# Optimization experiments

Measured on AMD Instinct MI355X. Metric: run time of the kernel, lower is better.

Reference implementation:

```python
import jax, jax.numpy as jnp
import numpy as np
from functools import partial

EPS = 1e-5
PATCH = 3
STYLE_STRENGTH = 1.0


def _whiten_color_mats(x):
    # x: (b, c, n) already flattened; returns mean, eigvecs, eigvals of covariance
    mean = x.mean(axis=-1, keepdims=True)
    xc = x - mean
    n = x.shape[-1]
    cov = jnp.einsum('bcn,bdn->bcd', xc, xc) / (n - 1)
    evals, evecs = jnp.linalg.eigh(cov)
    evals = jnp.maximum(evals, EPS)
    return mean, xc, evecs, evals


def whitening(x):
    b, c, h, w = x.shape
    xf = x.reshape(b, c, h * w)
    _, xc, E, d = _whiten_color_mats(xf)
    # W = E diag(d^-1/2) E^T
    Wm = jnp.einsum('bce,be,bde->bcd', E, d ** -0.5, E)
    return jnp.einsum('bcd,bdn->bcn', Wm, xc).reshape(b, c, h, w)


def coloring(x, style):
    b, c, h, w = x.shape
    xf = x.reshape(b, c, h * w)
    sf = style.reshape(b, c, -1)
    smean, sc, E, d = _whiten_color_mats(sf)
    Cm = jnp.einsum('bce,be,bde->bcd', E, d ** 0.5, E)
    out = jnp.einsum('bcd,bdn->bcn', Cm, xf) + smean
    return out.reshape(b, c, h, w)


def extract_style_kernels(style):
    # returns (b, hw, c, 3, 3) patches and (b, hw, 1, 1, 1) L2 norms
    b, c, H, W = style.shape
    p = jnp.pad(style, ((0, 0), (0, 0), (1, 1), (1, 1)), mode='reflect')
    patches = jnp.stack([p[:, :, i:i + H, j:j + W]
                         for i in range(PATCH) for j in range(PATCH)], axis=-1)  # (b,c,H,W,9)
    k = patches.reshape(b, c, H * W, PATCH * PATCH).transpose(0, 2, 1, 3)  # (b,hw,c,9)
    norm = jnp.sqrt(jnp.sum(k * k, axis=(2, 3))) + EPS  # (b,hw)
    return k.reshape(b, H * W, c, PATCH, PATCH), norm[:, :, None, None, None]


_DN = ('NCHW', 'OIHW', 'NCHW')


def _conv_per_sample(feat, kern):
    # feat (c,H,W), kern (o,c,3,3): reflect-pad 1, VALID conv -> (o,H,W)
    fp = jnp.pad(feat, ((0, 0), (1, 1), (1, 1)), mode='reflect')
    out = jax.lax.conv_general_dilated(fp[None], kern, (1, 1), 'VALID',
                                       dimension_numbers=_DN)
    return out[0]


def _deconv_per_sample(onehot, kern):
    # conv_transpose2d(stride=1, padding=2) == VALID conv with flipped, transposed kernel
    kt = jnp.flip(kern, axis=(-2, -1)).transpose(1, 0, 2, 3)  # (c, hw, 3, 3)
    fp = jnp.pad(onehot, ((0, 0), (1, 1), (1, 1)), mode='reflect')
    out = jax.lax.conv_general_dilated(fp[None], kt, (1, 1), 'VALID',
                                       dimension_numbers=_DN)
    return out[0]


def norm_deconvolution(h, w, patch_size):
    full = np.zeros((h + patch_size - 1, w + patch_size - 1), dtype=np.float32)
    for x in range(patch_size):
        for y in range(patch_size):
            full[y:y + h, x:x + w] += 1.0
    pw = (patch_size - 1) // 2
    if pw > 0:
        full = full[pw:-pw, pw:-pw]
    return jnp.asarray(full)[None, None]  # (1,1,h,w)


def reassemble_feature(nc, ns):
    b, c, H, W = nc.shape
    hw = H * W
    kern, norm = extract_style_kernels(ns)
    score = jax.vmap(_conv_per_sample)(nc, kern / norm)  # (b, hw, H, W)
    idx = jnp.argmax(score, axis=1)  # (b, H, W)
    onehot = (jnp.arange(hw, dtype=idx.dtype)[None, :, None, None] == idx[:, None]
              ).astype(nc.dtype)  # (b, hw, H, W)
    recon = jax.vmap(_deconv_per_sample)(onehot, kern)  # (b, c, H, W)
    return recon / norm_deconvolution(H, W, PATCH).astype(recon.dtype)


def setup_inputs() -> dict:
    key = jax.random.key(0)
    k1, k2 = jax.random.split(key)
    content_feature = jax.random.normal(k1, (2, 256, 64, 64), dtype=jnp.float32)
    style_feature = jax.random.normal(k2, (2, 256, 64, 64), dtype=jnp.float32)
    return {"content_feature": content_feature, "style_feature": style_feature}


def reference(content_feature, style_feature):
    nc = whitening(content_feature)
    ns = whitening(style_feature)
    reassembled = reassemble_feature(nc, ns)
    stylized = coloring(reassembled, style_feature)
    return (1.0 - STYLE_STRENGTH) * content_feature + STYLE_STRENGTH * stylized
```

## Files before the change

### kernel.cpp

```cpp
#include <hip/hip_runtime.h>
#include <hip/hip_bf16.h>

#define C_ 256
#define N_ 4096
#define CN (C_*N_)
#define EPSF 1e-5f
#define NS_ITERS 6
#define KSPLIT 16
#define LSTR 40

typedef _Float16 f16x8 __attribute__((ext_vector_type(8)));
typedef float f32x4 __attribute__((ext_vector_type(4)));

__device__ __forceinline__ int refl(int t) {
  return t < 0 ? -t : (t > 63 ? 126 - t : t);
}

__device__ __forceinline__ unsigned short f2h(float x) {
  _Float16 h = (_Float16)x;
  return __builtin_bit_cast(unsigned short, h);
}
__device__ __forceinline__ float h2f(unsigned short u) {
  return (float)__builtin_bit_cast(_Float16, u);
}

__device__ __forceinline__ void mm64_3term(unsigned short* sm, const float* A, const float* B,
                                           int m0, int n0, f32x4 acc[2][2]) {
  const int P = 64*LSTR;
  int t = threadIdx.x;
  int lane = t & 63;
  int wv = (t >> 7) & 1, wu = (t >> 6) & 1;
  int lx16 = lane & 15, quad = lane >> 4;
  int srow = t >> 2, sseg = (t & 3) * 8;
#pragma unroll
  for (int i = 0; i < 2; i++)
#pragma unroll
    for (int j = 0; j < 2; j++) acc[i][j] = (f32x4){0.f, 0.f, 0.f, 0.f};
  for (int k0 = 0; k0 < 256; k0 += 32) {
    __syncthreads();
    {
      const float* pa = &A[(size_t)(m0 + srow)*256 + k0 + sseg];
      const float* pb = &B[(size_t)(n0 + srow)*256 + k0 + sseg];
#pragma unroll
      for (int g = 0; g < 2; g++) {
        float4 va = *(const float4*)(pa + g*4);
        float4 vb = *(const float4*)(pb + g*4);
        float fa[4] = {va.x, va.y, va.z, va.w};
        float fb[4] = {vb.x, vb.y, vb.z, vb.w};
        unsigned short ha[4], la[4], hb[4], lb[4];
#pragma unroll
        for (int j = 0; j < 4; j++) {
          unsigned short h = f2h(fa[j]); ha[j] = h; la[j] = f2h(fa[j] - h2f(h));
          h = f2h(fb[j]); hb[j] = h; lb[j] = f2h(fb[j] - h2f(h));
        }
        int lo_ = srow*LSTR + sseg + g*4;
        *(ushort4*)&sm[0*P + lo_] = make_ushort4(ha[0], ha[1], ha[2], ha[3]);
        *(ushort4*)&sm[1*P + lo_] = make_ushort4(la[0], la[1], la[2], la[3]);
        *(ushort4*)&sm[2*P + lo_] = make_ushort4(hb[0], hb[1], hb[2], hb[3]);
        *(ushort4*)&sm[3*P + lo_] = make_ushort4(lb[0], lb[1], lb[2], lb[3]);
      }
    }
    __syncthreads();
    f16x8 ah[2], al[2], bh[2], bl[2];
#pragma unroll
    for (int mt = 0; mt < 2; mt++) {
      int arow = (wv*32 + mt*16 + lx16)*LSTR + quad*8;
      ah[mt] = *(const f16x8*)&sm[0*P + arow];
      al[mt] = *(const f16x8*)&sm[1*P + arow];
    }
#pragma unroll
    for (int nt = 0; nt < 2; nt++) {
      int brow = (wu*32 + nt*16 + lx16)*LSTR + quad*8;
      bh[nt] = *(const f16x8*)&sm[2*P + brow];
      bl[nt] = *(const f16x8*)&sm[3*P + brow];
    }
#pragma unroll
    for (int mt = 0; mt < 2; mt++)
#pragma unroll
      for (int nt = 0; nt < 2; nt++) {
        f32x4 a = acc[mt][nt];
        a = __builtin_amdgcn_mfma_f32_16x16x32_f16(ah[mt], bh[nt], a, 0, 0, 0);
        a = __builtin_amdgcn_mfma_f32_16x16x32_f16(ah[mt], bl[nt], a, 0, 0, 0);
        a = __builtin_amdgcn_mfma_f32_16x16x32_f16(al[mt], bh[nt], a, 0, 0, 0);
        acc[mt][nt] = a;
      }
  }
}

__device__ __forceinline__ f32x4 mm32_3term(unsigned short* sm, const float* A, const float* B,
                                            int m0, int n0) {
  const int P = 32*LSTR;
  int t = threadIdx.x, lane = t & 63;
  int w = t >> 6, wv = w >> 1, wu = w & 1;
  int lx16 = lane & 15, quad = lane >> 4;
  int mat = t >> 7, srow = (t >> 2) & 31, sseg = (t & 3) * 8;
  const float* S = mat ? B : A;
  int rb = mat ? n0 : m0;
  int base0 = mat ? 2*P : 0;
  f32x4 acc = (f32x4){0.f, 0.f, 0.f, 0.f};
  for (int k0 = 0; k0 < 256; k0 += 32) {
    __syncthreads();
    {
      const float* p = &S[(size_t)(rb + srow)*256 + k0 + sseg];
      int lo_ = srow*LSTR + sseg;
#pragma unroll
      for (int g = 0; g < 2; g++) {
        float4 v = *(const float4*)(p + g*4);
        float f[4] = {v.x, v.y, v.z, v.w};
        unsigned short hh[4], ll[4];
#pragma unroll
        for (int j = 0; j < 4; j++) {
          unsigned short h = f2h(f[j]); hh[j] = h; ll[j] = f2h(f[j] - h2f(h));
        }
        *(ushort4*)&sm[base0 + lo_ + g*4]     = make_ushort4(hh[0], hh[1], hh[2], hh[3]);
        *(ushort4*)&sm[base0 + P + lo_ + g*4] = make_ushort4(ll[0], ll[1], ll[2], ll[3]);
      }
    }
    __syncthreads();
    int arow = (wv*16 + lx16)*LSTR + quad*8;
    int brow = (wu*16 + lx16)*LSTR + quad*8;
    f16x8 ah = *(const f16x8*)&sm[0*P + arow];
    f16x8 al = *(const f16x8*)&sm[1*P + arow];
    f16x8 bh = *(const f16x8*)&sm[2*P + brow];
    f16x8 bl = *(const f16x8*)&sm[3*P + brow];
    acc = __builtin_amdgcn_mfma_f32_16x16x32_f16(ah, bh, acc, 0, 0, 0);
    acc = __builtin_amdgcn_mfma_f32_16x16x32_f16(ah, bl, acc, 0, 0, 0);
    acc = __builtin_amdgcn_mfma_f32_16x16x32_f16(al, bh, acc, 0, 0, 0);
  }
  return acc;
}

__global__ __launch_bounds__(256) void k_mean(const float* content, const float* style,
                                              float* means) {
  int c = blockIdx.x, m = blockIdx.y, t = threadIdx.x;
  const float* x = (m < 2 ? content : style) + (size_t)(m & 1) * CN + (size_t)c * N_;
  float s = 0.f;
  for (int i = t; i < N_; i += 256) s += x[i];
  __shared__ float red[256];
  red[t] = s; __syncthreads();
  for (int off = 128; off > 0; off >>= 1) { if (t < off) red[t] += red[t + off]; __syncthreads(); }
  if (t == 0) means[m * C_ + c] = red[0] * (1.f / N_);
}

__global__ __launch_bounds__(256) void k_splitall(const float* content, const float* style,
                                                  const float* means,
                                                  unsigned short* covsp, unsigned short* xcT) {
  int m = blockIdx.z;
  const float* x = (m < 2 ? content : style) + (size_t)(m & 1) * CN;
  int u0 = blockIdx.x * 32, c0 = blockIdx.y * 32;
  unsigned short* ch_ = covsp + (size_t)(2*m+0)*CN;
  unsigned short* cl_ = covsp + (size_t)(2*m+1)*CN;
  unsigned short* th_ = xcT + (size_t)(2*m+0)*CN;
  unsigned short* tl_ = xcT + (size_t)(2*m+1)*CN;
  __shared__ float tile[32][33];
  int t = threadIdx.x;
  {
    int cc = t >> 3, uu4 = (t & 7) * 4;
    float4 v = *(const float4*)&x[(size_t)(c0+cc)*N_ + u0 + uu4];
    float f[4] = {v.x, v.y, v.z, v.w};
    unsigned short h[4], lo[4];
#pragma unroll
    for (int j = 0; j < 4; j++) {
      unsigned short hh = f2h(f[j]);
      h[j] = hh; lo[j] = f2h(f[j] - h2f(hh));
      tile[cc][uu4+j] = f[j];
    }
    size_t o = (size_t)(c0+cc)*N_ + u0 + uu4;
    *(ushort4*)&ch_[o] = make_ushort4(h[0], h[1], h[2], h[3]);
    *(ushort4*)&cl_[o] = make_ushort4(lo[0], lo[1], lo[2], lo[3]);
  }
  __syncthreads();
  {
    int uu = t >> 3, cc4 = (t & 7) * 4;
    unsigned short h[4], lo[4];
#pragma unroll
    for (int j = 0; j < 4; j++) {
      float v = tile[cc4+j][uu] - means[m*C_ + c0 + cc4 + j];
      unsigned short hh = f2h(v);
      h[j] = hh; lo[j] = f2h(v - h2f(hh));
    }
    size_t o = (size_t)(u0+uu)*C_ + c0 + cc4;
    *(ushort4*)&th_[o] = make_ushort4(h[0], h[1], h[2], h[3]);
    *(ushort4*)&tl_[o] = make_ushort4(lo[0], lo[1], lo[2], lo[3]);
  }
}

__global__ __launch_bounds__(512) void k_covmm(const unsigned short* sp, float* covp) {
  __shared__ unsigned short sm[4*128*LSTR];
  const int P = 128*LSTR;
  int t = threadIdx.x;
  int kc = blockIdx.x, m = blockIdx.z;
  int ti = blockIdx.y >> 1, tj = blockIdx.y & 1;
  const unsigned short* Xh = sp + (size_t)m * 2 * (size_t)CN;
  const unsigned short* Xl = Xh + CN;
  int v0 = ti * 128, u0 = tj * 128;
  int wave = t >> 6, lane = t & 63;
  int wv = wave >> 1, wu = wave & 1;
  int lx16 = lane & 15, quad = lane >> 4;
  int srow = t >> 2, sseg = (t & 3) * 8;
  f32x4 acc[2][4];
#pragma unroll
  for (int i = 0; i < 2; i++)
#pragma unroll
    for (int j = 0; j < 4; j++) acc[i][j] = (f32x4){0.f, 0.f, 0.f, 0.f};

  int kbeg = kc * (N_ / KSPLIT), kend = kbeg + (N_ / KSPLIT);
  for (int k0 = kbeg; k0 < kend; k0 += 32) {
    __syncthreads();
    {
      size_t goA = (size_t)(v0 + srow) * N_ + k0 + sseg;
      size_t goB = (size_t)(u0 + srow) * N_ + k0 + sseg;
      int lo_ = srow * LSTR + sseg;
      *(float4*)&sm[0*P + lo_] = *(const float4*)&Xh[goA];
      *(float4*)&sm[1*P + lo_] = *(const float4*)&Xl[goA];
      *(float4*)&sm[2*P + lo_] = *(const float4*)&Xh[goB];
      *(float4*)&sm[3*P + lo_] = *(const float4*)&Xl[goB];
    }
    __syncthreads();
#pragma unroll
    for (int mt = 0; mt < 2; mt++) {
      int arow = (wv*32 + mt*16 + lx16)*LSTR + quad*8;
      f16x8 ah = *(const f16x8*)&sm[0*P + arow];
      f16x8 al = *(const f16x8*)&sm[1*P + arow];
#pragma unroll
      for (int nt = 0; nt < 4; nt++) {
        int brow = (wu*64 + nt*16 + lx16)*LSTR + quad*8;
        f16x8 bh = *(const f16x8*)&sm[2*P + brow];
        f16x8 bl = *(const f16x8*)&sm[3*P + brow];
        f32x4 a = acc[mt][nt];
        a = __builtin_amdgcn_mfma_f32_16x16x32_f16(ah, bh, a, 0, 0, 0);
        a = __builtin_amdgcn_mfma_f32_16x16x32_f16(ah, bl, a, 0, 0, 0);
        a = __builtin_amdgcn_mfma_f32_16x16x32_f16(al, bh, a, 0, 0, 0);
        acc[mt][nt] = a;
      }
    }
  }
  float* O = covp + ((size_t)kc*4 + m) * 65536;
#pragma unroll
  for (int mt = 0; mt < 2; mt++)
#pragma unroll
    for (int nt = 0; nt < 4; nt++)
#pragma unroll
      for (int i = 0; i < 4; i++)
        O[(size_t)(v0 + wv*32 + mt*16 + quad*4 + i)*C_ + (u0 + wu*64 + nt*16 + lx16)] =
            acc[mt][nt][i];
}

__global__ __launch_bounds__(256) void k_trace2(const float* covp, const float* means,
                                                float* cnrm) {
  int m = blockIdx.x, t = threadIdx.x;
  float s = 0.f;
#pragma unroll
  for (int kc = 0; kc < KSPLIT; kc++)
    s += covp[((size_t)kc*4 + m)*65536 + (size_t)t*257];
  float mi = means[m*C_ + t];
  float d = (s - (float)N_*mi*mi) * (1.f/(float)(N_-1));
  __shared__ float red[256];
  red[t] = d; __syncthreads();
  for (int off = 128; off > 0; off >>= 1) { if (t < off) red[t] += red[t + off]; __syncthreads(); }
  if (!t) cnrm[m] = red[0] * (1.3f/256.f);
}

__global__ __launch_bounds__(256) void k_covred_init(const float* covp, const float* means,
                                                     const float* cnrm, float* Y, float* Z) {
  int i = blockIdx.x, m = blockIdx.y, j = threadIdx.x;
  float s = 0.f;
#pragma unroll
  for (int kc = 0; kc < KSPLIT; kc++)
    s += covp[((size_t)kc*4 + m)*65536 + (size_t)i*C_ + j];
  float mi = means[m*C_ + i], mj = means[m*C_ + j];
  float cv = (s - (float)N_*mi*mj) * (1.f/(float)(N_-1));
  size_t o = (size_t)m*65536 + (size_t)i*C_ + j;
  Y[o] = cv / cnrm[m];
  Z[o] = (i == j) ? 1.f : 0.f;
}

__global__ __launch_bounds__(256) void k_nsA(const float* Zin, const float* Yin, float* T) {
  __shared__ unsigned short sm[4*32*LSTR];
  int m = blockIdx.y;
  int m0 = (blockIdx.x >> 3) * 32, n0 = (blockIdx.x & 7) * 32;
  const float* A = Zin + (size_t)m*65536;
  const float* B = Yin + (size_t)m*65536;
  float* O = T + (size_t)m*65536;
  f32x4 acc = mm32_3term(sm, A, B, m0, n0);
  int t = threadIdx.x, lane = t & 63;
  int w = t >> 6, wv = w >> 1, wu = w & 1;
  int lx16 = lane & 15, quad = lane >> 4;
#pragma unroll
  for (int i = 0; i < 4; i++) {
    int r = m0 + wv*16 + quad*4 + i;
    int c = n0 + wu*16 + lx16;
    float v = acc[i];
    O[(size_t)r*256 + c] = (r == c) ? 3.f - v : -v;
  }
}

__global__ __launch_bounds__(256) void k_nsB(const float* Yin, const float* Zin, const float* T,
                                             float* Yout, float* Zout) {
  __shared__ unsigned short sm[4*32*LSTR];
  int m = blockIdx.y, z = blockIdx.z;
  const float* A = (z == 0 ? Yin : Zin) + (size_t)m*65536;
  const float* B = T + (size_t)m*65536;
  float* O = (z == 0 ? Yout : Zout) + (size_t)m*65536;
  int m0 = (blockIdx.x >> 3) * 32, n0 = (blockIdx.x & 7) * 32;
  f32x4 acc = mm32_3term(sm, A, B, m0, n0);
  int t = threadIdx.x, lane = t & 63;
  int w = t >> 6, wv = w >> 1, wu = w & 1;
  int lx16 = lane & 15, quad = lane >> 4;
#pragma unroll
  for (int i = 0; i < 4; i++) {
    int r = m0 + wv*16 + quad*4 + i;
    int c = n0 + wu*16 + lx16;
    O[(size_t)r*256 + c] = 0.5f * acc[i];
  }
}

__global__ __launch_bounds__(256) void k_whitenT(const unsigned short* xcT, const float* Zall,
                                                 const float* cnrm, unsigned short* outT) {
  __shared__ unsigned short sm[4*64*LSTR];
  const int P = 64*LSTR;
  int m = blockIdx.z;
  int v0 = blockIdx.x * 64, c0 = blockIdx.y * 64;
  const float* Zm = Zall + (size_t)m*65536;
  const unsigned short* Bh_g = xcT + (size_t)(2*m+0)*CN;
  const unsigned short* Bl_g = xcT + (size_t)(2*m+1)*CN;
  unsigned short* Oh = outT + (size_t)(2*m+0)*CN;
  unsigned short* Ol = outT + (size_t)(2*m+1)*CN;
  int t = threadIdx.x, lane = t & 63;
  int wv = (t >> 7) & 1, wu = (t >> 6) & 1;
  int lx16 = lane & 15, quad = lane >> 4;
  int srow = t >> 2, sseg = (t & 3) * 8;
  f32x4 acc[2][2];
#pragma unroll
  for (int i = 0; i < 2; i++)
#pragma unroll
    for (int j = 0; j < 2; j++) acc[i][j] = (f32x4){0.f, 0.f, 0.f, 0.f};
  for (int k0 = 0; k0 < 256; k0 += 32) {
    __syncthreads();
    {
      const float* pa = &Zm[(size_t)(c0 + srow)*256 + k0 + sseg];
      int lo_ = srow*LSTR + sseg;
#pragma unroll
      for (int g = 0; g < 2; g++) {
        float4 va = *(const float4*)(pa + g*4);
        float fa[4] = {va.x, va.y, va.z, va.w};
        unsigned short ha[4], la[4];
#pragma unroll
        for (int j = 0; j < 4; j++) {
          unsigned short h = f2h(fa[j]); ha[j] = h; la[j] = f2h(fa[j] - h2f(h));
        }
        *(ushort4*)&sm[0*P + lo_ + g*4] = make_ushort4(ha[0], ha[1], ha[2], ha[3]);
        *(ushort4*)&sm[1*P + lo_ + g*4] = make_ushort4(la[0], la[1], la[2], la[3]);
      }
      size_t gb = (size_t)(v0 + srow)*C_ + k0 + sseg;
      *(float4*)&sm[2*P + lo_] = *(const float4*)&Bh_g[gb];
      *(float4*)&sm[3*P + lo_] = *(const float4*)&Bl_g[gb];
    }
    __syncthreads();
    f16x8 ah[2], al[2], bh[2], bl[2];
#pragma unroll
    for (int mt = 0; mt < 2; mt++) {
      int arow = (wv*32 + mt*16 + lx16)*LSTR + quad*8;
      ah[mt] = *(const f16x8*)&sm[0*P + arow];
      al[mt] = *(const f16x8*)&sm[1*P + arow];
    }
#pragma unroll
    for (int nt = 0; nt < 2; nt++) {
      int brow = (wu*32 + nt*16 + lx16)*LSTR + quad*8;
      bh[nt] = *(const f16x8*)&sm[2*P + brow];
      bl[nt] = *(const f16x8*)&sm[3*P + brow];
    }
#pragma unroll
    for (int mt = 0; mt < 2; mt++)
#pragma unroll
      for (int nt = 0; nt < 2; nt++) {
        f32x4 a = acc[mt][nt];
        a = __builtin_amdgcn_mfma_f32_16x16x32_f16(ah[mt], bh[nt], a, 0, 0, 0);
        a = __builtin_amdgcn_mfma_f32_16x16x32_f16(ah[mt], bl[nt], a, 0, 0, 0);
        a = __builtin_amdgcn_mfma_f32_16x16x32_f16(al[mt], bh[nt], a, 0, 0, 0);
        acc[mt][nt] = a;
      }
  }
  float scale = 1.0f / sqrtf(cnrm[m]);
  __syncthreads();
  unsigned short* Th = sm;
  unsigned short* Tl = sm + 64*72;
#pragma unroll
  for (int mt = 0; mt < 2; mt++)
#pragma unroll
    for (int nt = 0; nt < 2; nt++)
#pragma unroll
      for (int i = 0; i < 4; i++) {
        int chl = wv*32 + mt*16 + quad*4 + i;
        int vl  = wu*32 + nt*16 + lx16;
        float w = acc[mt][nt][i] * scale;
        unsigned short h = f2h(w);
        unsigned short l = f2h(w - h2f(h));
        Th[vl*72 + chl] = h;
        Tl[vl*72 + chl] = l;
      }
  __syncthreads();
  int vr = t >> 2, cs = (t & 3) * 16;
  size_t go = (size_t)(v0 + vr)*C_ + c0 + cs;
  *(float4*)&Oh[go]     = *(float4*)&Th[vr*72 + cs];
  *(float4*)&Oh[go + 8] = *(float4*)&Th[vr*72 + cs + 8];
  *(float4*)&Ol[go]     = *(float4*)&Tl[vr*72 + cs];
  *(float4*)&Ol[go + 8] = *(float4*)&Tl[vr*72 + cs + 8];
}

__global__ __launch_bounds__(256) void k_ssq(const unsigned short* outT, float* ssq) {
  int b = blockIdx.y; int p = blockIdx.x * 256 + threadIdx.x;
  const unsigned short* h = outT + (size_t)(2*(2+b))*CN + (size_t)p*C_;
  const unsigned short* l = h + CN;
  float acc = 0.f;
  for (int c = 0; c < C_; c += 4) {
    ushort4 hv = *(const ushort4*)&h[c];
    ushort4 lv = *(const ushort4*)&l[c];
    float v0 = h2f(hv.x) + h2f(lv.x);
    float v1 = h2f(hv.y) + h2f(lv.y);
    float v2 = h2f(hv.z) + h2f(lv.z);
    float v3 = h2f(hv.w) + h2f(lv.w);
    acc += v0*v0 + v1*v1 + v2*v2 + v3*v3;
  }
  ssq[b*N_ + p] = acc;
}

__global__ __launch_bounds__(256) void k_rnorm(const float* ssq, float* rnorm) {
  int b = blockIdx.y; int s = blockIdx.x * 256 + threadIdx.x;
  int sy = s >> 6, sx = s & 63;
  float sum = 0.f;
#pragma unroll
  for (int ky = 0; ky < 3; ky++)
#pragma unroll
    for (int kx = 0; kx < 3; kx++)
      sum += ssq[b*N_ + refl(sy+ky-1)*64 + refl(sx+kx-1)];
  rnorm[b*N_ + s] = 1.f / (sqrtf(sum) + EPSF);
}

__global__ __launch_bounds__(512) void k_gram(const unsigned short* Ah_g, const unsigned short* Al_g,
                                              const unsigned short* Bh_g, const unsigned short* Bl_g,
                                              float* Hx) {
  __shared__ unsigned short sm[4*128*LSTR];
  const int P = 128*LSTR;
  int t = threadIdx.x;
  int v0 = blockIdx.y * 128, u0 = blockIdx.x * 128;
  int wave = t >> 6, lane = t & 63;
  int wv = wave >> 1, wu = wave & 1;
  int lx16 = lane & 15, quad = lane >> 4;
  int srow = t >> 2, sseg = (t & 3) * 8;
  f32x4 acc[2][4];
#pragma unroll
  for (int i = 0; i < 2; i++)
#pragma unroll
    for (int j = 0; j < 4; j++) acc[i][j] = (f32x4){0.f, 0.f, 0.f, 0.f};

  for (int k0 = 0; k0 < 256; k0 += 32) {
    __syncthreads();
    {
      size_t goA = (size_t)(v0 + srow)*C_ + k0 + sseg;
      size_t goB = (size_t)(u0 + srow)*C_ + k0 + sseg;
      int lo_ = srow*LSTR + sseg;
      *(float4*)&sm[0*P + lo_] = *(const float4*)&Ah_g[goA];
      *(float4*)&sm[1*P + lo_] = *(const float4*)&Al_g[goA];
      *(float4*)&sm[2*P + lo_] = *(const float4*)&Bh_g[goB];
      *(float4*)&sm[3*P + lo_] = *(const float4*)&Bl_g[goB];
    }
    __syncthreads();
    int kb = quad*8;
    f16x8 ah[2], al[2];
#pragma unroll
    for (int mt = 0; mt < 2; mt++) {
      int arow = (wv*32 + mt*16 + lx16)*LSTR + kb;
      ah[mt] = *(const f16x8*)&sm[0*P + arow];
      al[mt] = *(const f16x8*)&sm[1*P + arow];
    }
    f16x8 bh[4], bl[4];
#pragma unroll
    for (int nt = 0; nt < 4; nt++) {
      int brow = (wu*64 + nt*16 + lx16)*LSTR + kb;
      bh[nt] = *(const f16x8*)&sm[2*P + brow];
      bl[nt] = *(const f16x8*)&sm[3*P + brow];
    }
#pragma unroll
    for (int mt = 0; mt < 2; mt++)
#pragma unroll
      for (int nt = 0; nt < 4; nt++) {
        f32x4 a = acc[mt][nt];
        a = __builtin_amdgcn_mfma_f32_16x16x32_f16(ah[mt], bh[nt], a, 0, 0, 0);
        a = __builtin_amdgcn_mfma_f32_16x16x32_f16(ah[mt], bl[nt], a, 0, 0, 0);
        a = __builtin_amdgcn_mfma_f32_16x16x32_f16(al[mt], bh[nt], a, 0, 0, 0);
        acc[mt][nt] = a;
      }
  }
  float* Gs = (float*)sm;
  int btx = t & 15, bty = t >> 4;
#pragma unroll
  for (int h = 0; h < 2; h++) {
    __syncthreads();
    if ((wv >> 1) == h) {
      int rbase = (wv & 1) * 32;
#pragma unroll
      for (int mt = 0; mt < 2; mt++)
#pragma unroll
        for (int nt = 0; nt < 4; nt++)
#pragma unroll
          for (int i = 0; i < 4; i++)
            Gs[(rbase + mt*16 + quad*4 + i)*133 + wu*64 + nt*16 + lx16] = acc[mt][nt][i];
    }
    __syncthreads();
#pragma unroll
    for (int i = 0; i < 2; i++) {
      int px = bty + 32*i;
      int xm = refl(px-1), xp = refl(px+1);
#pragma unroll
      for (int jh = 0; jh < 2; jh++) {
        int ub = jh*64;
        float tmp[4];
#pragma unroll
        for (int j = 0; j < 4; j++) {
          int sx = btx*4 + j;
          int smm = refl(sx-1), sp = refl(sx+1);
          tmp[j] = Gs[xm*133 + ub + smm] + Gs[px*133 + ub + sx] + Gs[xp*133 + ub + sp];
        }
        *(float4*)&Hx[(size_t)(v0 + h*64 + px)*N_ + u0 + ub + btx*4] =
            make_float4(tmp[0], tmp[1], tmp[2], tmp[3]);
      }
    }
  }
}

__global__ __launch_bounds__(256) void k_argmax(const float* Hx, const float* rnorm,
                                                int* idx, int b) {
  int blk = blockIdx.x, t = threadIdx.x;
  int q = blk >> 6, px = blk & 63;
  int py0 = 2*q, py1 = 2*q + 1;
  size_t rm = (size_t)(refl(py0-1)*64 + px) * N_;
  size_t r0 = (size_t)(py0*64 + px) * N_;
  size_t r1 = (size_t)(py1*64 + px) * N_;
  size_t rp = (size_t)(refl(py1+1)*64 + px) * N_;
  float bv0 = -1e30f, bv1 = -1e30f; int bs0 = 0, bs1 = 0;
  for (int s = t; s < N_; s += 256) {
    int sy = s >> 6, sx = s & 63;
    int u0 = refl(sy-1)*64 + sx, u2 = refl(sy+1)*64 + sx;
    float rn = rnorm[b*N_ + s];
    float a0 = Hx[rm + u0] + Hx[r0 + s] + Hx[r1 + u2];
    float a1 = Hx[r0 + u0] + Hx[r1 + s] + Hx[rp + u2];
    float sc0 = a0 * rn, sc1 = a1 * rn;
    if (sc0 > bv0) { bv0 = sc0; bs0 = s; }
    if (sc1 > bv1) { bv1 = sc1; bs1 = s; }
  }
  __shared__ float sv[256]; __shared__ int si[256];
  sv[t] = bv0; si[t] = bs0; __syncthreads();
  for (int off = 128; off > 0; off >>= 1) {
    if (t < off) {
      if (sv[t+off] > sv[t] || (sv[t+off] == sv[t] && si[t+off] < si[t])) {
        sv[t] = sv[t+off]; si[t] = si[t+off];
      }
    }
    __syncthreads();
  }
  if (!t) idx[b*N_ + py0*64 + px] = si[0];
  __syncthreads();
  sv[t] = bv1; si[t] = bs1; __syncthreads();
  for (int off = 128; off > 0; off >>= 1) {
    if (t < off) {
      if (sv[t+off] > sv[t] || (sv[t+off] == sv[t] && si[t+off] < si[t])) {
        sv[t] = sv[t+off]; si[t] = si[t+off];
      }
    }
    __syncthreads();
  }
  if (!t) idx[b*N_ + py1*64 + px] = si[0];
}

__global__ __launch_bounds__(256) void k_recon(const unsigned short* nsTh,
                                               const unsigned short* nsTl,
                                               const int* idx_b, float* recont_b) {
  int p = blockIdx.x, c = threadIdx.x;
  int py = p >> 6, px = p & 63;
  float acc = 0.f;
#pragma unroll
  for (int dy = 0; dy < 3; dy++)
#pragma unroll
    for (int dx = 0; dx < 3; dx++) {
      int q = refl(py+dy-1)*64 + refl(px+dx-1);
      int s = idx_b[q];
      int sy = s >> 6, sx = s & 63;
      size_t o = (size_t)(refl(sy+1-dy)*64 + refl(sx+1-dx))*C_ + c;
      acc += h2f(nsTh[o]) + h2f(nsTl[o]);
    }
  float dc = ((py==0||py==63)?2.f:3.f) * ((px==0||px==63)?2.f:3.f);
  recont_b[(size_t)p*C_ + c] = acc / dc;
}

__global__ __launch_bounds__(256) void k_color(const float* Yall, const float* recont_all,
                                               const float* cnrm, const float* means,
                                               float* out_all) {
  __shared__ unsigned short sm[4*64*LSTR];
  int b = blockIdx.z;
  const float* Ym = Yall + (size_t)(2+b)*65536;
  const float* recont = recont_all + (size_t)b*CN;
  const float* smean = means + (2+b)*C_;
  float* out = out_all + (size_t)b*CN;
  int m0 = blockIdx.y * 64;
  int n0 = blockIdx.x * 64;
  f32x4 acc[2][2];
  mm64_3term(sm, Ym, recont, m0, n0, acc);
  float scale = sqrtf(cnrm[2+b]);
  int t = threadIdx.x, lane = t & 63;
  int wv = (t >> 7) & 1, wu = (t >> 6) & 1, lx16 = lane & 15, quad = lane >> 4;
#pragma unroll
  for (int mt = 0; mt < 2; mt++)
#pragma unroll
    for (int nt = 0; nt < 2; nt++)
#pragma unroll
      for (int i = 0; i < 4; i++) {
        int r = m0 + wv*32 + mt*16 + quad*4 + i;
        int c = n0 + wu*32 + nt*16 + lx16;
        out[(size_t)r*N_ + c] = acc[mt][nt][i]*scale + smean[r];
      }
}

extern "C" void kernel_launch(void* const* d_in, const int* in_sizes, int n_in,
                              void* d_out, int out_size, void* d_ws, size_t ws_size,
                              hipStream_t stream) {
  const float* content = (const float*)d_in[0];
  const float* style   = (const float*)d_in[1];
  float* out = (float*)d_out;

  float* F = (float*)d_ws;
  float* means  = F + 0;
  float* cnrm   = F + 1024;
  float* Y      = F + 264192;
  float* Z      = F + 526336;
  float* Y2     = F + 788480;
  float* Z2     = F + 1050624;
  float* T      = F + 1312768;
  float* ncreg  = F + 1574912;
  float* nsreg  = F + 3672064;
  float* recont = F + 7866368;
  float* ssq    = F + 9963520;
  float* rnorm  = F + 9971712;
  int*   idx    = (int*)(F + 9979904);
  float* Hx     = F + 9988096;

  unsigned short* covsp = (unsigned short*)Hx;
  float* covp = Hx + 4194304;

  unsigned short* xcT  = (unsigned short*)nsreg;
  unsigned short* outT = (unsigned short*)ncreg;

  k_mean<<<dim3(256,4), 256, 0, stream>>>(content, style, means);
  k_splitall<<<dim3(128,8,4), 256, 0, stream>>>(content, style, means, covsp, xcT);
  k_covmm<<<dim3(KSPLIT,4,4), 512, 0, stream>>>(covsp, covp);
  k_trace2<<<4, 256, 0, stream>>>(covp, means, cnrm);
  k_covred_init<<<dim3(256,4), 256, 0, stream>>>(covp, means, cnrm, Y, Z);
  float *Ya = Y, *Za = Z, *Yb = Y2, *Zb = Z2;
  for (int it = 0; it < NS_ITERS; it++) {
    k_nsA<<<dim3(64,4), 256, 0, stream>>>(Za, Ya, T);
    k_nsB<<<dim3(64,4,2), 256, 0, stream>>>(Ya, Za, T, Yb, Zb);
    float* tmp;
    tmp = Ya; Ya = Yb; Yb = tmp;
    tmp = Za; Za = Zb; Zb = tmp;
  }
  k_whitenT<<<dim3(64,4,4), 256, 0, stream>>>(xcT, Za, cnrm, outT);
  k_ssq<<<dim3(16,2), 256, 0, stream>>>(outT, ssq);
  k_rnorm<<<dim3(16,2), 256, 0, stream>>>(ssq, rnorm);
  for (int b = 0; b < 2; b++) {
    k_gram<<<dim3(32,32), 512, 0, stream>>>(outT + (size_t)(2*b)*CN,
                                            outT + (size_t)(2*b+1)*CN,
                                            outT + (size_t)(2*(2+b))*CN,
                                            outT + (size_t)(2*(2+b)+1)*CN, Hx);
    k_argmax<<<2048, 256, 0, stream>>>(Hx, rnorm, idx, b);
    k_recon<<<4096, 256, 0, stream>>>(outT + (size_t)(2*(2+b))*CN,
                                      outT + (size_t)(2*(2+b)+1)*CN,
                                      idx + (size_t)b*N_, recont + (size_t)b*CN);
  }
  k_color<<<dim3(64,4,2), 256, 0, stream>>>(Ya, recont, cnrm, means, out);
}
```

Before: 351.8 us.

## Fuse Newton-Schulz iterations into cooperative kernel and widen argmax rows per block

Replaces the per-iteration Newton-Schulz kernel launches with one cooperative kernel that uses grid-wide syncs between phases. The argmax kernel now handles four output rows per block, so Hx rows shared between neighbours are reused. The covariance split-K factor is doubled and the mean kernel reads float4. The aim is less launch overhead and less redundant memory traffic. The cost is grid-sync overhead and a reliance on cooperative launch residency.

```diff
diff --git a/kernel.cpp b/kernel.cpp
--- a/kernel.cpp
+++ b/kernel.cpp
@@ -1,12 +1,15 @@
 #include <hip/hip_runtime.h>
 #include <hip/hip_bf16.h>
+#include <hip/hip_cooperative_groups.h>
+
+namespace cg = cooperative_groups;
 
 #define C_ 256
 #define N_ 4096
 #define CN (C_*N_)
 #define EPSF 1e-5f
 #define NS_ITERS 6
-#define KSPLIT 16
+#define KSPLIT 32
 #define LSTR 40
 
 typedef _Float16 f16x8 __attribute__((ext_vector_type(8)));
@@ -134,8 +137,13 @@
                                               float* means) {
   int c = blockIdx.x, m = blockIdx.y, t = threadIdx.x;
   const float* x = (m < 2 ? content : style) + (size_t)(m & 1) * CN + (size_t)c * N_;
+  const float4* x4 = (const float4*)x;
   float s = 0.f;
-  for (int i = t; i < N_; i += 256) s += x[i];
+#pragma unroll
+  for (int i = 0; i < 4; i++) {
+    float4 v = x4[t + i*256];
+    s += v.x + v.y + v.z + v.w;
+  }
   __shared__ float red[256];
   red[t] = s; __syncthreads();
   for (int off = 128; off > 0; off >>= 1) { if (t < off) red[t] += red[t + off]; __syncthreads(); }
@@ -275,43 +283,48 @@
   Z[o] = (i == j) ? 1.f : 0.f;
 }
 
-__global__ __launch_bounds__(256) void k_nsA(const float* Zin, const float* Yin, float* T) {
+__global__ __launch_bounds__(256) void k_ns_all(float* Y, float* Z, float* Y2, float* Z2,
+                                                float* T) {
+  cg::grid_group grid = cg::this_grid();
   __shared__ unsigned short sm[4*32*LSTR];
-  int m = blockIdx.y;
-  int m0 = (blockIdx.x >> 3) * 32, n0 = (blockIdx.x & 7) * 32;
-  const float* A = Zin + (size_t)m*65536;
-  const float* B = Yin + (size_t)m*65536;
-  float* O = T + (size_t)m*65536;
-  f32x4 acc = mm32_3term(sm, A, B, m0, n0);
+  int b = blockIdx.x;
   int t = threadIdx.x, lane = t & 63;
   int w = t >> 6, wv = w >> 1, wu = w & 1;
   int lx16 = lane & 15, quad = lane >> 4;
-#pragma unroll
-  for (int i = 0; i < 4; i++) {
-    int r = m0 + wv*16 + quad*4 + i;
-    int c = n0 + wu*16 + lx16;
-    float v = acc[i];
-    O[(size_t)r*256 + c] = (r == c) ? 3.f - v : -v;
-  }
-}
-
-__global__ __launch_bounds__(256) void k_nsB(const float* Yin, const float* Zin, const float* T,
-                                             float* Yout, float* Zout) {
-  __shared__ unsigned short sm[4*32*LSTR];
-  int m = blockIdx.y, z = blockIdx.z;
-  const float* A = (z == 0 ? Yin : Zin) + (size_t)m*65536;
-  const float* B = T + (size_t)m*65536;
-  float* O = (z == 0 ? Yout : Zout) + (size_t)m*65536;
-  int m0 = (blockIdx.x >> 3) * 32, n0 = (blockIdx.x & 7) * 32;
-  f32x4 acc = mm32_3term(sm, A, B, m0, n0);
-  int t = threadIdx.x, lane = t & 63;
-  int w = t >> 6, wv = w >> 1, wu = w & 1;
-  int lx16 = lane & 15, quad = lane >> 4;
-#pragma unroll
-  for (int i = 0; i < 4; i++) {
-    int r = m0 + wv*16 + quad*4 + i;
-    int c = n0 + wu*16 + lx16;
-    O[(size_t)r*256 + c] = 0.5f * acc[i];
+  float *Ya = Y, *Za = Z, *Yb = Y2, *Zb = Z2;
+  for (int it = 0; it < NS_ITERS; it++) {
+    {
+      int m = b >> 6, tile = b & 63;
+      int m0 = (tile >> 3) * 32, n0 = (tile & 7) * 32;
+      f32x4 acc = mm32_3term(sm, Za + (size_t)m*65536, Ya + (size_t)m*65536, m0, n0);
+      float* O = T + (size_t)m*65536;
+#pragma unroll
+      for (int i = 0; i < 4; i++) {
+        int r = m0 + wv*16 + quad*4 + i;
+        int c = n0 + wu*16 + lx16;
+        float v = acc[i];
+        O[(size_t)r*256 + c] = (r == c) ? 3.f - v : -v;
+      }
+    }
+    grid.sync();
+    for (int j = 0; j < 2; j++) {
+      int idx2 = b*2 + j;
+      int m = idx2 >> 7, rem = idx2 & 127, z = rem >> 6, tile = rem & 63;
+      int m0 = (tile >> 3) * 32, n0 = (tile & 7) * 32;
+      const float* A = (z == 0 ? Ya : Za) + (size_t)m*65536;
+      f32x4 acc = mm32_3term(sm, A, T + (size_t)m*65536, m0, n0);
+      float* O = (z == 0 ? Yb : Zb) + (size_t)m*65536;
+#pragma unroll
+      for (int i = 0; i < 4; i++) {
+        int r = m0 + wv*16 + quad*4 + i;
+        int c = n0 + wu*16 + lx16;
+        O[(size_t)r*256 + c] = 0.5f * acc[i];
+      }
+    }
+    grid.sync();
+    float* tmp;
+    tmp = Ya; Ya = Yb; Yb = tmp;
+    tmp = Za; Za = Zb; Zb = tmp;
   }
 }
 
@@ -393,9 +406,9 @@
       for (int i = 0; i < 4; i++) {
         int chl = wv*32 + mt*16 + quad*4 + i;
         int vl  = wu*32 + nt*16 + lx16;
-        float w = acc[mt][nt][i] * scale;
-        unsigned short h = f2h(w);
-        unsigned short l = f2h(w - h2f(h));
+        float ww = acc[mt][nt][i] * scale;
+        unsigned short h = f2h(ww);
+        unsigned short l = f2h(ww - h2f(h));
         Th[vl*72 + chl] = h;
         Tl[vl*72 + chl] = l;
       }
@@ -533,44 +546,40 @@
                                                 int* idx, int b) {
   int blk = blockIdx.x, t = threadIdx.x;
   int q = blk >> 6, px = blk & 63;
-  int py0 = 2*q, py1 = 2*q + 1;
-  size_t rm = (size_t)(refl(py0-1)*64 + px) * N_;
-  size_t r0 = (size_t)(py0*64 + px) * N_;
-  size_t r1 = (size_t)(py1*64 + px) * N_;
-  size_t rp = (size_t)(refl(py1+1)*64 + px) * N_;
-  float bv0 = -1e30f, bv1 = -1e30f; int bs0 = 0, bs1 = 0;
+  int py0 = 4*q;
+  size_t R[6];
+  R[0] = (size_t)(refl(py0-1)*64 + px) * N_;
+#pragma unroll
+  for (int j = 0; j < 4; j++) R[j+1] = (size_t)((py0+j)*64 + px) * N_;
+  R[5] = (size_t)(refl(py0+4)*64 + px) * N_;
+  float bv[4] = {-1e30f, -1e30f, -1e30f, -1e30f};
+  int bs[4] = {0, 0, 0, 0};
   for (int s = t; s < N_; s += 256) {
     int sy = s >> 6, sx = s & 63;
     int u0 = refl(sy-1)*64 + sx, u2 = refl(sy+1)*64 + sx;
     float rn = rnorm[b*N_ + s];
-    float a0 = Hx[rm + u0] + Hx[r0 + s] + Hx[r1 + u2];
-    float a1 = Hx[r0 + u0] + Hx[r1 + s] + Hx[rp + u2];
-    float sc0 = a0 * rn, sc1 = a1 * rn;
-    if (sc0 > bv0) { bv0 = sc0; bs0 = s; }
-    if (sc1 > bv1) { bv1 = sc1; bs1 = s; }
+#pragma unroll
+    for (int j = 0; j < 4; j++) {
+      float a = Hx[R[j] + u0] + Hx[R[j+1] + s] + Hx[R[j+2] + u2];
+      float sc = a * rn;
+      if (sc > bv[j]) { bv[j] = sc; bs[j] = s; }
+    }
   }
   __shared__ float sv[256]; __shared__ int si[256];
-  sv[t] = bv0; si[t] = bs0; __syncthreads();
-  for (int off = 128; off > 0; off >>= 1) {
-    if (t < off) {
-      if (sv[t+off] > sv[t] || (sv[t+off] == sv[t] && si[t+off] < si[t])) {
-        sv[t] = sv[t+off]; si[t] = si[t+off];
-      }
-    }
-    __syncthreads();
-  }
-  if (!t) idx[b*N_ + py0*64 + px] = si[0];
-  __syncthreads();
-  sv[t] = bv1; si[t] = bs1; __syncthreads();
-  for (int off = 128; off > 0; off >>= 1) {
-    if (t < off) {
-      if (sv[t+off] > sv[t] || (sv[t+off] == sv[t] && si[t+off] < si[t])) {
-        sv[t] = sv[t+off]; si[t] = si[t+off];
-      }
-    }
-    __syncthreads();
-  }
-  if (!t) idx[b*N_ + py1*64 + px] = si[0];
+#pragma unroll
+  for (int j = 0; j < 4; j++) {
+    __syncthreads();
+    sv[t] = bv[j]; si[t] = bs[j]; __syncthreads();
+    for (int off = 128; off > 0; off >>= 1) {
+      if (t < off) {
+        if (sv[t+off] > sv[t] || (sv[t+off] == sv[t] && si[t+off] < si[t])) {
+          sv[t] = sv[t+off]; si[t] = si[t+off];
+        }
+      }
+      __syncthreads();
+    }
+    if (!t) idx[b*N_ + (py0+j)*64 + px] = si[0];
+  }
 }
 
 __global__ __launch_bounds__(256) void k_recon(const unsigned short* nsTh,
@@ -655,15 +664,11 @@
   k_covmm<<<dim3(KSPLIT,4,4), 512, 0, stream>>>(covsp, covp);
   k_trace2<<<4, 256, 0, stream>>>(covp, means, cnrm);
   k_covred_init<<<dim3(256,4), 256, 0, stream>>>(covp, means, cnrm, Y, Z);
-  float *Ya = Y, *Za = Z, *Yb = Y2, *Zb = Z2;
-  for (int it = 0; it < NS_ITERS; it++) {
-    k_nsA<<<dim3(64,4), 256, 0, stream>>>(Za, Ya, T);
-    k_nsB<<<dim3(64,4,2), 256, 0, stream>>>(Ya, Za, T, Yb, Zb);
-    float* tmp;
-    tmp = Ya; Ya = Yb; Yb = tmp;
-    tmp = Za; Za = Zb; Zb = tmp;
-  }
-  k_whitenT<<<dim3(64,4,4), 256, 0, stream>>>(xcT, Za, cnrm, outT);
+  {
+    void* args[] = {(void*)&Y, (void*)&Z, (void*)&Y2, (void*)&Z2, (void*)&T};
+    hipLaunchCooperativeKernel((const void*)k_ns_all, dim3(256), dim3(256), args, 0, stream);
+  }
+  k_whitenT<<<dim3(64,4,4), 256, 0, stream>>>(xcT, Z, cnrm, outT);
   k_ssq<<<dim3(16,2), 256, 0, stream>>>(outT, ssq);
   k_rnorm<<<dim3(16,2), 256, 0, stream>>>(ssq, rnorm);
   for (int b = 0; b < 2; b++) {
@@ -671,10 +676,10 @@
                                             outT + (size_t)(2*b+1)*CN,
                                             outT + (size_t)(2*(2+b))*CN,
                                             outT + (size_t)(2*(2+b)+1)*CN, Hx);
-    k_argmax<<<2048, 256, 0, stream>>>(Hx, rnorm, idx, b);
+    k_argmax<<<1024, 256, 0, stream>>>(Hx, rnorm, idx, b);
     k_recon<<<4096, 256, 0, stream>>>(outT + (size_t)(2*(2+b))*CN,
                                       outT + (size_t)(2*(2+b)+1)*CN,
                                       idx + (size_t)b*N_, recont + (size_t)b*CN);
   }
-  k_color<<<dim3(64,4,2), 256, 0, stream>>>(Ya, recont, cnrm, means, out);
-}
+  k_color<<<dim3(64,4,2), 256, 0, stream>>>(Y, recont, cnrm, means, out);
+}
```

After: 767.0 us. +118.0%, slower.
